# Kernel tuning notes

Measured on AMD Instinct MI355X. Metric: run time of the kernel, lower is better.

Reference implementation:

```python
import jax, jax.numpy as jnp
import numpy as np

NUM_HEADS = 8
KEY_DIM = 64
VALUE_DIM = 64
UPDATE_STEPS_MAX = 3
UPDATE_EPS = 1e-4
LN_EPS = 1e-5


def _layernorm(x, gamma, beta):
    # normalize over last axis (key_dim), per build: shape (..., num_heads, key_dim)
    mu = jnp.mean(x, axis=-1, keepdims=True)
    var = jnp.var(x, axis=-1, keepdims=True)
    return (x - mu) * jax.lax.rsqrt(var + LN_EPS) * gamma + beta


def setup_inputs() -> dict:
    key = jax.random.key(0)
    ks = jax.random.split(key, 8)
    D = 512
    B, S = 8, 1024
    s = 1.0 / np.sqrt(D)
    return {
        "x": jax.random.normal(ks[0], (B, S, D), jnp.float32),
        "Wq": jax.random.normal(ks[1], (D, NUM_HEADS * KEY_DIM), jnp.float32) * s,
        "bq": jnp.zeros((NUM_HEADS * KEY_DIM,), jnp.float32),
        "Wk": jax.random.normal(ks[2], (D, NUM_HEADS * KEY_DIM), jnp.float32) * s,
        "bk": jnp.zeros((NUM_HEADS * KEY_DIM,), jnp.float32),
        "Wv": jax.random.normal(ks[3], (D, NUM_HEADS * VALUE_DIM), jnp.float32) * s,
        "bv": jnp.zeros((NUM_HEADS * VALUE_DIM,), jnp.float32),
        "Wo": jax.random.normal(ks[4], (NUM_HEADS * VALUE_DIM, D), jnp.float32) * s,
        "bo": jnp.zeros((D,), jnp.float32),
        "gamma": jnp.ones((KEY_DIM,), jnp.float32),
        "beta": jnp.zeros((KEY_DIM,), jnp.float32),
    }


def reference(x, Wq, bq, Wk, bk, Wv, bv, Wo, bo, gamma, beta):
    B, S, D = x.shape
    H, dk, dv = NUM_HEADS, KEY_DIM, VALUE_DIM
    # QKV projections -> (B, S, H, d)
    q = (x @ Wq + bq).reshape(B, S, H, dk)
    k = (x @ Wk + bk).reshape(B, S, H, dk)
    v = (x @ Wv + bv).reshape(B, S, H, dv)
    # pattern normalization (LayerNorm over key_dim)
    q = _layernorm(q, gamma, beta)
    k = _layernorm(k, gamma, beta)
    # -> (B, H, S, d)
    q = q.transpose(0, 2, 1, 3)
    k = k.transpose(0, 2, 1, 3)
    v = v.transpose(0, 2, 1, 3)
    scale = jnp.sqrt(jnp.asarray(dk, q.dtype))
    # iterative Hopfield association updates: q <- softmax(qK^T/scale) K
    for _ in range(UPDATE_STEPS_MAX):
        attn = jax.nn.softmax(jnp.einsum("bhqd,bhkd->bhqk", q, k) / scale, axis=-1)
        new_q = jnp.einsum("bhqk,bhkd->bhqd", attn, k)
        diff = jnp.linalg.norm(new_q - q)
        q = jnp.where(diff > UPDATE_EPS, new_q, q)  # eps-gated update
    # final retrieval with values
    attn = jax.nn.softmax(jnp.einsum("bhqd,bhkd->bhqk", q, k) / scale, axis=-1)
    out = jnp.einsum("bhqk,bhkd->bhqd", attn, v)
    out = out.transpose(0, 2, 1, 3).reshape(B, S, H * dv)
    return out @ Wo + bo
```

## Files before the change

kernel.cpp:

```cpp
#include <hip/hip_runtime.h>
#include <stdint.h>


#define DEV static __device__ __forceinline__

typedef __attribute__((ext_vector_type(8))) short short8;
typedef __attribute__((ext_vector_type(8))) __bf16 bf16x8;
typedef __attribute__((ext_vector_type(4))) float f32x4;
typedef __attribute__((ext_vector_type(16))) float f32x16;
typedef __attribute__((ext_vector_type(4))) unsigned int uint4v;

DEV unsigned short f2bf(float f) {
  unsigned int u = __builtin_bit_cast(unsigned int, f);
  u = u + 0x7fffu + ((u >> 16) & 1u);
  return (unsigned short)(u >> 16);
}

DEV unsigned int cvtpk(float lo, float hi) {
  unsigned int r;
  asm("v_cvt_pk_bf16_f32 %0, %1, %2" : "=v"(r) : "v"(lo), "v"(hi));
  return r;
}

DEV f32x4 mfma16(short8 a, short8 b, f32x4 c) {
  return __builtin_amdgcn_mfma_f32_16x16x32_bf16(
      __builtin_bit_cast(bf16x8, a), __builtin_bit_cast(bf16x8, b), c, 0, 0, 0);
}

DEV f32x16 mfma32(short8 a, short8 b, f32x16 c) {
  return __builtin_amdgcn_mfma_f32_32x32x16_bf16(
      __builtin_bit_cast(bf16x8, a), __builtin_bit_cast(bf16x8, b), c, 0, 0, 0);
}

DEV f32x16 zero16() {
  f32x16 z;
#pragma unroll
  for (int i = 0; i < 16; ++i) z[i] = 0.f;
  return z;
}

DEV void gload16(void* lds, const void* g) {
  __builtin_amdgcn_global_load_lds(
      (const __attribute__((address_space(1))) void*)(uintptr_t)g,
      (__attribute__((address_space(3))) void*)(unsigned int)(uintptr_t)lds,
      16, 0, 0);
}

__global__ __launch_bounds__(256)
void xcast_kernel(const float* __restrict__ x, unsigned short* __restrict__ xbf) {
  int i = blockIdx.x * 256 + threadIdx.x;
  float4 v = ((const float4*)x)[i];
  ushort4 o;
  o.x = f2bf(v.x); o.y = f2bf(v.y); o.z = f2bf(v.z); o.w = f2bf(v.w);
  ((ushort4*)xbf)[i] = o;
}

__global__ __launch_bounds__(256)
void wtrans_kernel(const float* __restrict__ Wq, const float* __restrict__ Wk,
                   const float* __restrict__ Wv, const float* __restrict__ Wo,
                   unsigned short* __restrict__ wqkvT, unsigned short* __restrict__ woT) {
  __shared__ float t[64][65];
  int job = blockIdx.x;
  int wsel = job >> 6;
  int tile = job & 63;
  int tr = (tile >> 3) * 64;
  int tc = (tile & 7) * 64;
  const float* W = wsel == 0 ? Wq : wsel == 1 ? Wk : wsel == 2 ? Wv : Wo;
  unsigned short* T = wsel < 3 ? wqkvT + (size_t)wsel * 512 * 512 : woT;
  int lane = threadIdx.x & 63;
  int wv = threadIdx.x >> 6;
  for (int rr = 0; rr < 16; ++rr) {
    int r = wv * 16 + rr;
    t[r][lane] = W[(size_t)(tr + r) * 512 + tc + lane];
  }
  __syncthreads();
  for (int rr = 0; rr < 16; ++rr) {
    int r = wv * 16 + rr;
    T[(size_t)(tc + r) * 512 + tr + lane] = f2bf(t[lane][r]);
  }
}

template <int MODE>
__global__ __launch_bounds__(256, 2)
void gemm_kernel(const unsigned short* __restrict__ A,
                 const unsigned short* __restrict__ WT,
                 const float* __restrict__ b0, const float* __restrict__ b1,
                 const float* __restrict__ b2,
                 const float* __restrict__ gamma, const float* __restrict__ beta,
                 unsigned short* __restrict__ Qo, unsigned short* __restrict__ Ko,
                 unsigned short* __restrict__ Vo, float* __restrict__ Fo) {
  __shared__ __align__(16) unsigned char As[2][16384];
  __shared__ __align__(16) unsigned char Ws[2][16384];

  const int tid = threadIdx.x;
  const int lane = tid & 63;
  const int w = tid >> 6;
  const int l15 = lane & 15;
  const int l4 = lane >> 4;
  const int m0 = blockIdx.x * 128;
  const int by = blockIdx.y;
  const int wm = (w >> 1) * 64;
  const int wn = (w & 1) * 64;

  f32x4 acc[4][4];
#pragma unroll
  for (int mt = 0; mt < 4; ++mt)
#pragma unroll
    for (int nt = 0; nt < 4; ++nt) acc[mt][nt] = (f32x4){0.f, 0.f, 0.f, 0.f};

  auto stage = [&](int i) {
    int buf = i & 1;
    int k0 = i * 64;
#pragma unroll
    for (int it = 0; it < 4; ++it) {
      int idx = it * 256 + tid;
      int row = idx >> 3;
      int sc = ((idx & 7) * 16) ^ ((row & 7) << 4);
      gload16(As[buf] + idx * 16,
              (const unsigned char*)A + ((size_t)(m0 + row) * 512 + k0) * 2 + sc);
      gload16(Ws[buf] + idx * 16,
              (const unsigned char*)WT + ((size_t)(by * 128 + row) * 512 + k0) * 2 + sc);
    }
  };

  stage(0);
  __syncthreads();

  for (int i = 0; i < 8; ++i) {
    int buf = i & 1;
    if (i < 7) stage(i + 1);
    __builtin_amdgcn_s_setprio(1);
#pragma unroll
    for (int kk = 0; kk < 2; ++kk) {
      short8 af[4], bfr[4];
#pragma unroll
      for (int mt = 0; mt < 4; ++mt) {
        int row = wm + mt * 16 + l15;
        int colb = (l4 * 16 + kk * 64) ^ ((row & 7) << 4);
        af[mt] = *(const short8*)(As[buf] + row * 128 + colb);
      }
#pragma unroll
      for (int nt = 0; nt < 4; ++nt) {
        int row = wn + nt * 16 + l15;
        int colb = (l4 * 16 + kk * 64) ^ ((row & 7) << 4);
        bfr[nt] = *(const short8*)(Ws[buf] + row * 128 + colb);
      }
#pragma unroll
      for (int mt = 0; mt < 4; ++mt)
#pragma unroll
        for (int nt = 0; nt < 4; ++nt) acc[mt][nt] = mfma16(af[mt], bfr[nt], acc[mt][nt]);
    }
    __builtin_amdgcn_s_setprio(0);
    __syncthreads();
  }

  const float cs = 1.4426950408889634f / 8.0f;
  const float* bias = (MODE == 1) ? b0 : (by >> 2) == 0 ? b0 : (by >> 2) == 1 ? b1 : b2;
  float bvv[4];
#pragma unroll
  for (int nt = 0; nt < 4; ++nt) bvv[nt] = bias[(by & 3) * 128 + wn + nt * 16 + l15];

  if (MODE == 1) {
#pragma unroll
    for (int mt = 0; mt < 4; ++mt)
#pragma unroll
      for (int r = 0; r < 4; ++r) {
        int gr = m0 + wm + mt * 16 + l4 * 4 + r;
#pragma unroll
        for (int nt = 0; nt < 4; ++nt)
          Fo[(size_t)gr * 512 + (by & 3) * 128 + wn + nt * 16 + l15] =
              acc[mt][nt][r] + bvv[nt];
      }
  } else {
    const int seg = by >> 2;
    const int h = (by & 3) * 2 + (wn >> 6);
    if (seg == 2) {
#pragma unroll
      for (int mt = 0; mt < 4; ++mt)
#pragma unroll
        for (int r = 0; r < 4; ++r) {
          int gr = m0 + wm + mt * 16 + l4 * 4 + r;
          int b = gr >> 10, s = gr & 1023;
          size_t base = ((size_t)(b * 8 + h) << 16) + ((size_t)s << 6);
#pragma unroll
          for (int nt = 0; nt < 4; ++nt)
            Vo[base + nt * 16 + l15] = f2bf(acc[mt][nt][r] + bvv[nt]);
        }
    } else {
      float g4[4], be4[4];
#pragma unroll
      for (int nt = 0; nt < 4; ++nt) {
        g4[nt] = gamma[nt * 16 + l15];
        be4[nt] = beta[nt * 16 + l15];
      }
      unsigned short* dst = seg == 0 ? Qo : Ko;
      const float m = seg == 0 ? cs : 1.0f;
#pragma unroll
      for (int mt = 0; mt < 4; ++mt)
#pragma unroll
        for (int r = 0; r < 4; ++r) {
          float v[4];
#pragma unroll
          for (int nt = 0; nt < 4; ++nt) v[nt] = acc[mt][nt][r] + bvv[nt];
          float s1 = (v[0] + v[1]) + (v[2] + v[3]);
          s1 += __shfl_xor(s1, 1); s1 += __shfl_xor(s1, 2);
          s1 += __shfl_xor(s1, 4); s1 += __shfl_xor(s1, 8);
          float mu = s1 * (1.0f / 64.0f);
          float s2 = v[0]*v[0] + v[1]*v[1] + v[2]*v[2] + v[3]*v[3];
          s2 += __shfl_xor(s2, 1); s2 += __shfl_xor(s2, 2);
          s2 += __shfl_xor(s2, 4); s2 += __shfl_xor(s2, 8);
          float var = s2 * (1.0f / 64.0f) - mu * mu;
          float rs = rsqrtf(var + 1e-5f);
          int gr = m0 + wm + mt * 16 + l4 * 4 + r;
          int b = gr >> 10, s = gr & 1023;
          size_t base = ((size_t)(b * 8 + h) << 16) + ((size_t)s << 6);
#pragma unroll
          for (int nt = 0; nt < 4; ++nt) {
            float y = ((v[nt] - mu) * rs * g4[nt] + be4[nt]) * m;
            dst[base + nt * 16 + l15] = f2bf(y);
          }
        }
    }
  }
}

__global__ __launch_bounds__(256)
void ktrans_kernel(const unsigned short* __restrict__ Kb,
                   const unsigned short* __restrict__ Vb,
                   unsigned short* __restrict__ KTg, unsigned short* __restrict__ VTg) {
  __shared__ unsigned short tile[64][65];
  const int c = blockIdx.x;
  const int bh = blockIdx.y;
  const unsigned short* src = blockIdx.z ? Vb : Kb;
  unsigned short* dst = blockIdx.z ? VTg : KTg;
  const int t = threadIdx.x;
  {
    int j = t >> 2, c16 = (t & 3) * 16;
    const unsigned short* sp = src + ((size_t)bh << 16) + ((size_t)(c * 64 + j) << 6) + c16;
    unsigned short vals[16];
    *(uint4*)(vals) = *(const uint4*)(sp);
    *(uint4*)(vals + 8) = *(const uint4*)(sp + 8);
#pragma unroll
    for (int i = 0; i < 16; ++i) tile[j][c16 + i] = vals[i];
  }
  __syncthreads();
  {
    int d = t >> 2, k16 = (t & 3) * 16;
    unsigned short ov[16];
#pragma unroll
    for (int i = 0; i < 16; ++i) {
      int kp = k16 + i;
      int g = kp >> 5, r5 = kp & 31;
      int c16 = r5 >> 4, h = (r5 >> 3) & 1, ii = r5 & 7;
      int phys = g * 32 + c16 * 16 + 8 * (ii >> 2) + 4 * h + (ii & 3);
      ov[i] = tile[phys][d];
    }
    unsigned short* dp = dst + ((size_t)bh << 16) + ((size_t)d << 10) + c * 64 + k16;
    *(uint4*)(dp) = *(uint4*)(ov);
    *(uint4*)(dp + 8) = *(uint4*)(ov + 8);
  }
}

__global__ __launch_bounds__(256, 2)
void attn_kernel(const unsigned short* __restrict__ Qb,
                 const unsigned short* __restrict__ Kb,
                 const unsigned short* __restrict__ KTg,
                 const unsigned short* __restrict__ VTg,
                 unsigned short* __restrict__ Ob) {
  __shared__ __align__(16) unsigned char Kc[2][8192];
  __shared__ __align__(16) unsigned char Tc[2][8192];

  const int tid = threadIdx.x;
  const int lane = tid & 63;
  const int w = tid >> 6;
  const int l31 = lane & 31;
  const int hi = lane >> 5;
  const int bi = blockIdx.x;
  const int xcd = bi & 7, wnd = bi >> 3;
  const int bh = xcd * 8 + (wnd & 7);
  const int qt = wnd >> 3;
  const int q0 = qt * 128 + w * 32;
  const size_t kvb = (size_t)bh << 17;
  const float cs = 1.4426950408889634f / 8.0f;

  int sOffK[2], sOffT[2];
#pragma unroll
  for (int it = 0; it < 2; ++it) {
    int idx = it * 256 + tid;
    int row = idx >> 3;
    int colb = ((idx & 7) * 16) ^ ((row & 7) << 4);
    sOffK[it] = row * 128 + colb;
    sOffT[it] = row * 2048 + colb;
  }
  const unsigned char* kS = (const unsigned char*)Kb + kvb;
  const unsigned char* tKS = (const unsigned char*)KTg + kvb;
  const unsigned char* tVS = (const unsigned char*)VTg + kvb;

  auto stage = [&](int t) {
    int c = t & 15, buf = t & 1;
    const unsigned char* ts = (t >= 48) ? tVS : tKS;
#pragma unroll
    for (int it = 0; it < 2; ++it) {
      int idx = it * 256 + tid;
      gload16(Kc[buf] + idx * 16, kS + (size_t)c * 8192 + sOffK[it]);
      gload16(Tc[buf] + idx * 16, ts + (size_t)c * 128 + sOffT[it]);
    }
  };

  stage(0);

  short8 qf[4];
  {
    const unsigned char* qp =
        (const unsigned char*)Qb + kvb + ((size_t)(q0 + l31) << 7) + hi * 16;
    qf[0] = *(const short8*)(qp);
    qf[1] = *(const short8*)(qp + 32);
    qf[2] = *(const short8*)(qp + 64);
    qf[3] = *(const short8*)(qp + 96);
  }

  f32x16 acc0 = zero16(), acc1 = zero16();
  float lsum = 0.f;
  const int sw = (l31 & 7) << 4;
  const int hb = hi * 16;
  const int rowA = l31 * 128;

  auto compute = [&](int buf) {
    const unsigned char* KB = Kc[buf];
    const unsigned char* TB = Tc[buf];
    short8 kfa[4], kfb[4];
#pragma unroll
    for (int s = 0; s < 4; ++s) {
      int cb = (32 * s + hb) ^ sw;
      kfa[s] = *(const short8*)(KB + rowA + cb);
      kfb[s] = *(const short8*)(KB + 4096 + rowA + cb);
    }
    f32x16 s0 = zero16(), s1 = zero16();
    __builtin_amdgcn_s_setprio(1);
#pragma unroll
    for (int s = 0; s < 4; ++s) {
      s0 = mfma32(kfa[s], qf[s], s0);
      s1 = mfma32(kfb[s], qf[s], s1);
    }
    __builtin_amdgcn_s_setprio(0);
    unsigned int u0[8], u1[8];
#pragma unroll
    for (int r = 0; r < 16; r += 2) {
      float pA = exp2f(s0[r]), pB = exp2f(s0[r + 1]);
      lsum += pA + pB;
      u0[r >> 1] = cvtpk(pA, pB);
    }
#pragma unroll
    for (int r = 0; r < 16; r += 2) {
      float pA = exp2f(s1[r]), pB = exp2f(s1[r + 1]);
      lsum += pA + pB;
      u1[r >> 1] = cvtpk(pA, pB);
    }
    short8 p00 = __builtin_bit_cast(short8, (uint4v){u0[0], u0[1], u0[2], u0[3]});
    short8 p01 = __builtin_bit_cast(short8, (uint4v){u0[4], u0[5], u0[6], u0[7]});
    short8 p10 = __builtin_bit_cast(short8, (uint4v){u1[0], u1[1], u1[2], u1[3]});
    short8 p11 = __builtin_bit_cast(short8, (uint4v){u1[4], u1[5], u1[6], u1[7]});
    short8 t0, t1;
    __builtin_amdgcn_s_setprio(1);
    t0 = *(const short8*)(TB + rowA + ((0 + hb) ^ sw));
    t1 = *(const short8*)(TB + 4096 + rowA + ((0 + hb) ^ sw));
    acc0 = mfma32(t0, p00, acc0);
    acc1 = mfma32(t1, p00, acc1);
    t0 = *(const short8*)(TB + rowA + ((32 + hb) ^ sw));
    t1 = *(const short8*)(TB + 4096 + rowA + ((32 + hb) ^ sw));
    acc0 = mfma32(t0, p01, acc0);
    acc1 = mfma32(t1, p01, acc1);
    t0 = *(const short8*)(TB + rowA + ((64 + hb) ^ sw));
    t1 = *(const short8*)(TB + 4096 + rowA + ((64 + hb) ^ sw));
    acc0 = mfma32(t0, p10, acc0);
    acc1 = mfma32(t1, p10, acc1);
    t0 = *(const short8*)(TB + rowA + ((96 + hb) ^ sw));
    t1 = *(const short8*)(TB + 4096 + rowA + ((96 + hb) ^ sw));
    acc0 = mfma32(t0, p11, acc0);
    acc1 = mfma32(t1, p11, acc1);
    __builtin_amdgcn_s_setprio(0);
  };

  __syncthreads();

  for (int p = 0; p < 4; ++p) {
    for (int c2 = 0; c2 < 16; c2 += 2) {
      {
        int t = p * 16 + c2;
        if (t < 63) stage(t + 1);
        compute(0);
        __syncthreads();
      }
      {
        int t = p * 16 + c2 + 1;
        if (t < 63) stage(t + 1);
        compute(1);
        __syncthreads();
      }
    }
    lsum += __shfl_xor(lsum, 32);
    if (p < 3) {
      float f = cs / lsum;
#pragma unroll
      for (int s = 0; s < 4; ++s) {
        const f32x16& A = (s >> 1) ? acc1 : acc0;
        const int base = 8 * (s & 1);
        float a0 = A[base] * f, a1 = A[base + 1] * f;
        float a2 = A[base + 2] * f, a3 = A[base + 3] * f;
        float b0 = A[base + 4] * f, b1 = A[base + 5] * f;
        float b2 = A[base + 6] * f, b3 = A[base + 7] * f;
        float s0_ = hi ? a0 : b0, s1_ = hi ? a1 : b1;
        float s2_ = hi ? a2 : b2, s3_ = hi ? a3 : b3;
        float r0 = __shfl_xor(s0_, 32), r1 = __shfl_xor(s1_, 32);
        float r2 = __shfl_xor(s2_, 32), r3 = __shfl_xor(s3_, 32);
        float e0 = hi ? r0 : a0, e1 = hi ? r1 : a1;
        float e2 = hi ? r2 : a2, e3 = hi ? r3 : a3;
        float e4 = hi ? b0 : r0, e5 = hi ? b1 : r1;
        float e6 = hi ? b2 : r2, e7 = hi ? b3 : r3;
        qf[s] = __builtin_bit_cast(
            short8, (uint4v){cvtpk(e0, e1), cvtpk(e2, e3), cvtpk(e4, e5), cvtpk(e6, e7)});
      }
      acc0 = zero16();
      acc1 = zero16();
      lsum = 0.f;
    } else {
      float inv = 1.0f / lsum;
      const int b = bh >> 3, h = bh & 7;
      const int qg = q0 + l31;
      unsigned short* orow = Ob + ((size_t)(b * 1024 + qg) << 9) + h * 64;
#pragma unroll
      for (int dt = 0; dt < 2; ++dt) {
        const f32x16& A = dt ? acc1 : acc0;
#pragma unroll
        for (int rq = 0; rq < 4; ++rq) {
          ushort4 o;
          o.x = f2bf(A[4 * rq + 0] * inv);
          o.y = f2bf(A[4 * rq + 1] * inv);
          o.z = f2bf(A[4 * rq + 2] * inv);
          o.w = f2bf(A[4 * rq + 3] * inv);
          *(ushort4*)(orow + dt * 32 + 8 * rq + 4 * hi) = o;
        }
      }
    }
  }
}

extern "C" void kernel_launch(void* const* d_in, const int* in_sizes, int n_in,
                              void* d_out, int out_size, void* d_ws, size_t ws_size,
                              hipStream_t stream) {
  const float* x  = (const float*)d_in[0];
  const float* Wq = (const float*)d_in[1];
  const float* bq = (const float*)d_in[2];
  const float* Wk = (const float*)d_in[3];
  const float* bk = (const float*)d_in[4];
  const float* Wv = (const float*)d_in[5];
  const float* bv = (const float*)d_in[6];
  const float* Wo = (const float*)d_in[7];
  const float* bo = (const float*)d_in[8];
  const float* gamma = (const float*)d_in[9];
  const float* beta  = (const float*)d_in[10];
  (void)in_sizes; (void)n_in; (void)out_size; (void)ws_size;

  char* ws = (char*)d_ws;
  size_t off = 0;
  auto alloc = [&](size_t bytes) {
    char* p = ws + off;
    off += (bytes + 255) & ~(size_t)255;
    return p;
  };
  unsigned short* xbf   = (unsigned short*)alloc(8192ull * 512 * 2);
  unsigned short* wqkvT = (unsigned short*)alloc(1536ull * 512 * 2);
  unsigned short* woT   = (unsigned short*)alloc(512ull * 512 * 2);
  unsigned short* Qbf   = (unsigned short*)alloc(64ull * 1024 * 64 * 2);
  unsigned short* Kbf   = (unsigned short*)alloc(64ull * 1024 * 64 * 2);
  unsigned short* Vbf   = (unsigned short*)alloc(64ull * 1024 * 64 * 2);
  unsigned short* KTg   = (unsigned short*)alloc(64ull * 1024 * 64 * 2);
  unsigned short* VTg   = (unsigned short*)alloc(64ull * 1024 * 64 * 2);
  unsigned short* Obf   = (unsigned short*)alloc(8192ull * 512 * 2);

  xcast_kernel<<<4096, 256, 0, stream>>>(x, xbf);
  wtrans_kernel<<<256, 256, 0, stream>>>(Wq, Wk, Wv, Wo, wqkvT, woT);

  gemm_kernel<0><<<dim3(64, 12), 256, 0, stream>>>(
      xbf, wqkvT, bq, bk, bv, gamma, beta, Qbf, Kbf, Vbf, nullptr);

  ktrans_kernel<<<dim3(16, 64, 2), 256, 0, stream>>>(Kbf, Vbf, KTg, VTg);

  attn_kernel<<<512, 256, 0, stream>>>(Qbf, Kbf, KTg, VTg, Obf);

  gemm_kernel<1><<<dim3(64, 4), 256, 0, stream>>>(
      Obf, woT, bo, nullptr, nullptr, nullptr, nullptr,
      nullptr, nullptr, nullptr, (float*)d_out);
}
```

Before: 231.5 us.

## Deepen attention pipeline to prefetch two tiles ahead and software-pipeline PV

Measured after the change: 232.5 us. Within noise of the previous version (+0.4%).

```diff
diff --git a/kernel.cpp b/kernel.cpp
--- a/kernel.cpp
+++ b/kernel.cpp
@@ -267,8 +267,8 @@
                  const unsigned short* __restrict__ KTg,
                  const unsigned short* __restrict__ VTg,
                  unsigned short* __restrict__ Ob) {
-  __shared__ __align__(16) unsigned char Kc[2][8192];
-  __shared__ __align__(16) unsigned char Tc[2][8192];
+  __shared__ __align__(16) unsigned char Kc[3][8192];
+  __shared__ __align__(16) unsigned char Tc[4][8192];
 
   const int tid = threadIdx.x;
   const int lane = tid & 63;
@@ -297,17 +297,17 @@
   const unsigned char* tVS = (const unsigned char*)VTg + kvb;
 
   auto stage = [&](int t) {
-    int c = t & 15, buf = t & 1;
+    int c = t & 15;
     const unsigned char* ts = (t >= 48) ? tVS : tKS;
+    unsigned char* kd = Kc[t % 3];
+    unsigned char* td = Tc[t & 3];
 #pragma unroll
     for (int it = 0; it < 2; ++it) {
       int idx = it * 256 + tid;
-      gload16(Kc[buf] + idx * 16, kS + (size_t)c * 8192 + sOffK[it]);
-      gload16(Tc[buf] + idx * 16, ts + (size_t)c * 128 + sOffT[it]);
+      gload16(kd + idx * 16, kS + (size_t)c * 8192 + sOffK[it]);
+      gload16(td + idx * 16, ts + (size_t)c * 128 + sOffT[it]);
     }
   };
-
-  stage(0);
 
   short8 qf[4];
   {
@@ -319,128 +319,148 @@
     qf[3] = *(const short8*)(qp + 96);
   }
 
+  stage(0);
+  stage(1);
+  asm volatile("s_waitcnt vmcnt(4)" ::: "memory");
+  __builtin_amdgcn_s_barrier();
+  __builtin_amdgcn_sched_barrier(0);
+
   f32x16 acc0 = zero16(), acc1 = zero16();
   float lsum = 0.f;
   const int sw = (l31 & 7) << 4;
   const int hb = hi * 16;
   const int rowA = l31 * 128;
 
-  auto compute = [&](int buf) {
-    const unsigned char* KB = Kc[buf];
-    const unsigned char* TB = Tc[buf];
-    short8 kfa[4], kfb[4];
-#pragma unroll
-    for (int s = 0; s < 4; ++s) {
-      int cb = (32 * s + hb) ^ sw;
-      kfa[s] = *(const short8*)(KB + rowA + cb);
-      kfb[s] = *(const short8*)(KB + 4096 + rowA + cb);
-    }
-    f32x16 s0 = zero16(), s1 = zero16();
-    __builtin_amdgcn_s_setprio(1);
-#pragma unroll
-    for (int s = 0; s < 4; ++s) {
-      s0 = mfma32(kfa[s], qf[s], s0);
-      s1 = mfma32(kfb[s], qf[s], s1);
-    }
-    __builtin_amdgcn_s_setprio(0);
-    unsigned int u0[8], u1[8];
-#pragma unroll
-    for (int r = 0; r < 16; r += 2) {
-      float pA = exp2f(s0[r]), pB = exp2f(s0[r + 1]);
-      lsum += pA + pB;
-      u0[r >> 1] = cvtpk(pA, pB);
-    }
-#pragma unroll
-    for (int r = 0; r < 16; r += 2) {
-      float pA = exp2f(s1[r]), pB = exp2f(s1[r + 1]);
-      lsum += pA + pB;
-      u1[r >> 1] = cvtpk(pA, pB);
-    }
-    short8 p00 = __builtin_bit_cast(short8, (uint4v){u0[0], u0[1], u0[2], u0[3]});
-    short8 p01 = __builtin_bit_cast(short8, (uint4v){u0[4], u0[5], u0[6], u0[7]});
-    short8 p10 = __builtin_bit_cast(short8, (uint4v){u1[0], u1[1], u1[2], u1[3]});
-    short8 p11 = __builtin_bit_cast(short8, (uint4v){u1[4], u1[5], u1[6], u1[7]});
+  short8 p0, p1, p2, p3;
+
+  auto PV = [&](int bufT) {
+    const unsigned char* TB = Tc[bufT];
     short8 t0, t1;
-    __builtin_amdgcn_s_setprio(1);
     t0 = *(const short8*)(TB + rowA + ((0 + hb) ^ sw));
     t1 = *(const short8*)(TB + 4096 + rowA + ((0 + hb) ^ sw));
-    acc0 = mfma32(t0, p00, acc0);
-    acc1 = mfma32(t1, p00, acc1);
+    acc0 = mfma32(t0, p0, acc0);
+    acc1 = mfma32(t1, p0, acc1);
     t0 = *(const short8*)(TB + rowA + ((32 + hb) ^ sw));
     t1 = *(const short8*)(TB + 4096 + rowA + ((32 + hb) ^ sw));
-    acc0 = mfma32(t0, p01, acc0);
-    acc1 = mfma32(t1, p01, acc1);
+    acc0 = mfma32(t0, p1, acc0);
+    acc1 = mfma32(t1, p1, acc1);
     t0 = *(const short8*)(TB + rowA + ((64 + hb) ^ sw));
     t1 = *(const short8*)(TB + 4096 + rowA + ((64 + hb) ^ sw));
-    acc0 = mfma32(t0, p10, acc0);
-    acc1 = mfma32(t1, p10, acc1);
+    acc0 = mfma32(t0, p2, acc0);
+    acc1 = mfma32(t1, p2, acc1);
     t0 = *(const short8*)(TB + rowA + ((96 + hb) ^ sw));
     t1 = *(const short8*)(TB + 4096 + rowA + ((96 + hb) ^ sw));
-    acc0 = mfma32(t0, p11, acc0);
-    acc1 = mfma32(t1, p11, acc1);
-    __builtin_amdgcn_s_setprio(0);
+    acc0 = mfma32(t0, p3, acc0);
+    acc1 = mfma32(t1, p3, acc1);
   };
 
-  __syncthreads();
-
-  for (int p = 0; p < 4; ++p) {
-    for (int c2 = 0; c2 < 16; c2 += 2) {
-      {
-        int t = p * 16 + c2;
-        if (t < 63) stage(t + 1);
-        compute(0);
-        __syncthreads();
-      }
-      {
-        int t = p * 16 + c2 + 1;
-        if (t < 63) stage(t + 1);
-        compute(1);
-        __syncthreads();
-      }
-    }
-    lsum += __shfl_xor(lsum, 32);
-    if (p < 3) {
-      float f = cs / lsum;
+  for (int t = 0; t < 64; ++t) {
+    const int c = t & 15;
+    if (t + 2 < 64) stage(t + 2);
+
+    f32x16 s0 = zero16(), s1 = zero16();
+    {
+      const unsigned char* KB = Kc[t % 3];
+      short8 kfa[4], kfb[4];
 #pragma unroll
       for (int s = 0; s < 4; ++s) {
-        const f32x16& A = (s >> 1) ? acc1 : acc0;
-        const int base = 8 * (s & 1);
-        float a0 = A[base] * f, a1 = A[base + 1] * f;
-        float a2 = A[base + 2] * f, a3 = A[base + 3] * f;
-        float b0 = A[base + 4] * f, b1 = A[base + 5] * f;
-        float b2 = A[base + 6] * f, b3 = A[base + 7] * f;
-        float s0_ = hi ? a0 : b0, s1_ = hi ? a1 : b1;
-        float s2_ = hi ? a2 : b2, s3_ = hi ? a3 : b3;
-        float r0 = __shfl_xor(s0_, 32), r1 = __shfl_xor(s1_, 32);
-        float r2 = __shfl_xor(s2_, 32), r3 = __shfl_xor(s3_, 32);
-        float e0 = hi ? r0 : a0, e1 = hi ? r1 : a1;
-        float e2 = hi ? r2 : a2, e3 = hi ? r3 : a3;
-        float e4 = hi ? b0 : r0, e5 = hi ? b1 : r1;
-        float e6 = hi ? b2 : r2, e7 = hi ? b3 : r3;
-        qf[s] = __builtin_bit_cast(
-            short8, (uint4v){cvtpk(e0, e1), cvtpk(e2, e3), cvtpk(e4, e5), cvtpk(e6, e7)});
-      }
-      acc0 = zero16();
-      acc1 = zero16();
-      lsum = 0.f;
-    } else {
-      float inv = 1.0f / lsum;
-      const int b = bh >> 3, h = bh & 7;
-      const int qg = q0 + l31;
-      unsigned short* orow = Ob + ((size_t)(b * 1024 + qg) << 9) + h * 64;
-#pragma unroll
-      for (int dt = 0; dt < 2; ++dt) {
-        const f32x16& A = dt ? acc1 : acc0;
-#pragma unroll
-        for (int rq = 0; rq < 4; ++rq) {
-          ushort4 o;
-          o.x = f2bf(A[4 * rq + 0] * inv);
-          o.y = f2bf(A[4 * rq + 1] * inv);
-          o.z = f2bf(A[4 * rq + 2] * inv);
-          o.w = f2bf(A[4 * rq + 3] * inv);
-          *(ushort4*)(orow + dt * 32 + 8 * rq + 4 * hi) = o;
+        int cb = (32 * s + hb) ^ sw;
+        kfa[s] = *(const short8*)(KB + rowA + cb);
+        kfb[s] = *(const short8*)(KB + 4096 + rowA + cb);
+      }
+      __builtin_amdgcn_s_setprio(1);
+#pragma unroll
+      for (int s = 0; s < 4; ++s) {
+        s0 = mfma32(kfa[s], qf[s], s0);
+        s1 = mfma32(kfb[s], qf[s], s1);
+      }
+      __builtin_amdgcn_s_setprio(0);
+    }
+
+    if (c > 0) {
+      __builtin_amdgcn_s_setprio(1);
+      PV((t - 1) & 3);
+      __builtin_amdgcn_s_setprio(0);
+    }
+
+    {
+      unsigned int u0[8], u1[8];
+#pragma unroll
+      for (int r = 0; r < 16; r += 2) {
+        float pA = exp2f(s0[r]), pB = exp2f(s0[r + 1]);
+        lsum += pA + pB;
+        u0[r >> 1] = cvtpk(pA, pB);
+      }
+#pragma unroll
+      for (int r = 0; r < 16; r += 2) {
+        float pA = exp2f(s1[r]), pB = exp2f(s1[r + 1]);
+        lsum += pA + pB;
+        u1[r >> 1] = cvtpk(pA, pB);
+      }
+      p0 = __builtin_bit_cast(short8, (uint4v){u0[0], u0[1], u0[2], u0[3]});
+      p1 = __builtin_bit_cast(short8, (uint4v){u0[4], u0[5], u0[6], u0[7]});
+      p2 = __builtin_bit_cast(short8, (uint4v){u1[0], u1[1], u1[2], u1[3]});
+      p3 = __builtin_bit_cast(short8, (uint4v){u1[4], u1[5], u1[6], u1[7]});
+    }
+
+    if (c == 15) {
+      __builtin_amdgcn_s_setprio(1);
+      PV(t & 3);
+      __builtin_amdgcn_s_setprio(0);
+      lsum += __shfl_xor(lsum, 32);
+      if (t < 63) {
+        float f = cs / lsum;
+#pragma unroll
+        for (int s = 0; s < 4; ++s) {
+          const f32x16& A = (s >> 1) ? acc1 : acc0;
+          const int base = 8 * (s & 1);
+          float a0 = A[base] * f, a1 = A[base + 1] * f;
+          float a2 = A[base + 2] * f, a3 = A[base + 3] * f;
+          float b0 = A[base + 4] * f, b1 = A[base + 5] * f;
+          float b2 = A[base + 6] * f, b3 = A[base + 7] * f;
+          float s0_ = hi ? a0 : b0, s1_ = hi ? a1 : b1;
+          float s2_ = hi ? a2 : b2, s3_ = hi ? a3 : b3;
+          float r0 = __shfl_xor(s0_, 32), r1 = __shfl_xor(s1_, 32);
+          float r2 = __shfl_xor(s2_, 32), r3 = __shfl_xor(s3_, 32);
+          float e0 = hi ? r0 : a0, e1 = hi ? r1 : a1;
+          float e2 = hi ? r2 : a2, e3 = hi ? r3 : a3;
+          float e4 = hi ? b0 : r0, e5 = hi ? b1 : r1;
+          float e6 = hi ? b2 : r2, e7 = hi ? b3 : r3;
+          qf[s] = __builtin_bit_cast(
+              short8, (uint4v){cvtpk(e0, e1), cvtpk(e2, e3), cvtpk(e4, e5), cvtpk(e6, e7)});
         }
-      }
+        acc0 = zero16();
+        acc1 = zero16();
+        lsum = 0.f;
+      } else {
+        float inv = 1.0f / lsum;
+        const int b = bh >> 3, h = bh & 7;
+        const int qg = q0 + l31;
+        unsigned short* orow = Ob + ((size_t)(b * 1024 + qg) << 9) + h * 64;
+#pragma unroll
+        for (int dt = 0; dt < 2; ++dt) {
+          const f32x16& A = dt ? acc1 : acc0;
+#pragma unroll
+          for (int rq = 0; rq < 4; ++rq) {
+            ushort4 o;
+            o.x = f2bf(A[4 * rq + 0] * inv);
+            o.y = f2bf(A[4 * rq + 1] * inv);
+            o.z = f2bf(A[4 * rq + 2] * inv);
+            o.w = f2bf(A[4 * rq + 3] * inv);
+            *(ushort4*)(orow + dt * 32 + 8 * rq + 4 * hi) = o;
+          }
+        }
+      }
+    }
+
+    if (t < 63) {
+      if (t == 62) {
+        asm volatile("s_waitcnt vmcnt(0)" ::: "memory");
+      } else {
+        asm volatile("s_waitcnt vmcnt(4)" ::: "memory");
+      }
+      __builtin_amdgcn_s_barrier();
+      __builtin_amdgcn_sched_barrier(0);
     }
   }
 }
```

## Load transposed K/V fragments directly from global into registers, stage K in big LDS halves

Applied to the files above, without the earlier changes.

Result: slower. 268.4 us (+16.0%).

```diff
diff --git a/kernel.cpp b/kernel.cpp
--- a/kernel.cpp
+++ b/kernel.cpp
@@ -44,6 +44,21 @@
       (const __attribute__((address_space(1))) void*)(uintptr_t)g,
       (__attribute__((address_space(3))) void*)(unsigned int)(uintptr_t)lds,
       16, 0, 0);
+}
+
+struct TFrag { short8 a0, a1, a2, a3, b0, b1, b2, b3; };
+
+DEV TFrag load_t(const unsigned char* p) {
+  TFrag f;
+  f.a0 = *(const short8*)(p);
+  f.a1 = *(const short8*)(p + 32);
+  f.a2 = *(const short8*)(p + 64);
+  f.a3 = *(const short8*)(p + 96);
+  f.b0 = *(const short8*)(p + 4096);
+  f.b1 = *(const short8*)(p + 4128);
+  f.b2 = *(const short8*)(p + 4160);
+  f.b3 = *(const short8*)(p + 4192);
+  return f;
 }
 
 __global__ __launch_bounds__(256)
@@ -227,12 +242,12 @@
 __global__ __launch_bounds__(256)
 void ktrans_kernel(const unsigned short* __restrict__ Kb,
                    const unsigned short* __restrict__ Vb,
-                   unsigned short* __restrict__ KTg, unsigned short* __restrict__ VTg) {
+                   unsigned short* __restrict__ KTc, unsigned short* __restrict__ VTc) {
   __shared__ unsigned short tile[64][65];
   const int c = blockIdx.x;
   const int bh = blockIdx.y;
   const unsigned short* src = blockIdx.z ? Vb : Kb;
-  unsigned short* dst = blockIdx.z ? VTg : KTg;
+  unsigned short* dst = blockIdx.z ? VTc : KTc;
   const int t = threadIdx.x;
   {
     int j = t >> 2, c16 = (t & 3) * 16;
@@ -255,7 +270,7 @@
       int phys = g * 32 + c16 * 16 + 8 * (ii >> 2) + 4 * h + (ii & 3);
       ov[i] = tile[phys][d];
     }
-    unsigned short* dp = dst + ((size_t)bh << 16) + ((size_t)d << 10) + c * 64 + k16;
+    unsigned short* dp = dst + ((size_t)bh << 16) + c * 4096 + d * 64 + k16;
     *(uint4*)(dp) = *(uint4*)(ov);
     *(uint4*)(dp + 8) = *(uint4*)(ov + 8);
   }
@@ -264,84 +279,79 @@
 __global__ __launch_bounds__(256, 2)
 void attn_kernel(const unsigned short* __restrict__ Qb,
                  const unsigned short* __restrict__ Kb,
-                 const unsigned short* __restrict__ KTg,
-                 const unsigned short* __restrict__ VTg,
+                 const unsigned short* __restrict__ KTc,
+                 const unsigned short* __restrict__ VTc,
                  unsigned short* __restrict__ Ob) {
-  __shared__ __align__(16) unsigned char Kc[2][8192];
-  __shared__ __align__(16) unsigned char Tc[2][8192];
+  __shared__ __align__(16) unsigned char Kc[65536];
 
   const int tid = threadIdx.x;
   const int lane = tid & 63;
   const int w = tid >> 6;
   const int l31 = lane & 31;
   const int hi = lane >> 5;
-  const int bi = blockIdx.x;
-  const int xcd = bi & 7, wnd = bi >> 3;
-  const int bh = xcd * 8 + (wnd & 7);
-  const int qt = wnd >> 3;
+  const int bid = blockIdx.x;
+  const int bh = (bid & 7) * 8 + ((bid >> 3) & 7);
+  const int qt = bid >> 6;
   const int q0 = qt * 128 + w * 32;
   const size_t kvb = (size_t)bh << 17;
   const float cs = 1.4426950408889634f / 8.0f;
 
-  int sOffK[2], sOffT[2];
-#pragma unroll
-  for (int it = 0; it < 2; ++it) {
-    int idx = it * 256 + tid;
-    int row = idx >> 3;
-    int colb = ((idx & 7) * 16) ^ ((row & 7) << 4);
-    sOffK[it] = row * 128 + colb;
-    sOffT[it] = row * 2048 + colb;
-  }
   const unsigned char* kS = (const unsigned char*)Kb + kvb;
-  const unsigned char* tKS = (const unsigned char*)KTg + kvb;
-  const unsigned char* tVS = (const unsigned char*)VTg + kvb;
-
-  auto stage = [&](int t) {
-    int c = t & 15, buf = t & 1;
-    const unsigned char* ts = (t >= 48) ? tVS : tKS;
-#pragma unroll
-    for (int it = 0; it < 2; ++it) {
+  const int tlane = l31 * 128 + hi * 16;
+  const unsigned char* tKl = (const unsigned char*)KTc + kvb + tlane;
+  const unsigned char* tVl = (const unsigned char*)VTc + kvb + tlane;
+
+  auto stageK = [&](int h) {
+    const unsigned char* s = kS + h * 65536;
+#pragma unroll
+    for (int it = 0; it < 16; ++it) {
       int idx = it * 256 + tid;
-      gload16(Kc[buf] + idx * 16, kS + (size_t)c * 8192 + sOffK[it]);
-      gload16(Tc[buf] + idx * 16, ts + (size_t)c * 128 + sOffT[it]);
+      int row = idx >> 3;
+      int colb = ((idx & 7) * 16) ^ ((row & 7) << 4);
+      gload16(Kc + idx * 16, s + row * 128 + colb);
     }
   };
 
-  stage(0);
-
+  const int sw = (l31 & 7) << 4;
+  const int hb = hi * 16;
+  const int rowA = l31 * 128;
+  const int ko0 = rowA + ((0 + hb) ^ sw);
+  const int ko1 = rowA + ((32 + hb) ^ sw);
+  const int ko2 = rowA + ((64 + hb) ^ sw);
+  const int ko3 = rowA + ((96 + hb) ^ sw);
+
+  stageK(0);
   short8 qf[4];
   {
     const unsigned char* qp =
-        (const unsigned char*)Qb + kvb + ((size_t)(q0 + l31) << 7) + hi * 16;
+        (const unsigned char*)Qb + kvb + (size_t)(q0 + l31) * 128 + hb;
     qf[0] = *(const short8*)(qp);
     qf[1] = *(const short8*)(qp + 32);
     qf[2] = *(const short8*)(qp + 64);
     qf[3] = *(const short8*)(qp + 96);
   }
+  asm volatile("s_waitcnt vmcnt(0)" ::: "memory");
+  __builtin_amdgcn_s_barrier();
 
   f32x16 acc0 = zero16(), acc1 = zero16();
   float lsum = 0.f;
-  const int sw = (l31 & 7) << 4;
-  const int hb = hi * 16;
-  const int rowA = l31 * 128;
-
-  auto compute = [&](int buf) {
-    const unsigned char* KB = Kc[buf];
-    const unsigned char* TB = Tc[buf];
-    short8 kfa[4], kfb[4];
-#pragma unroll
-    for (int s = 0; s < 4; ++s) {
-      int cb = (32 * s + hb) ^ sw;
-      kfa[s] = *(const short8*)(KB + rowA + cb);
-      kfb[s] = *(const short8*)(KB + 4096 + rowA + cb);
-    }
+  TFrag tA = load_t(tKl), tB;
+
+  auto compute = [&](int cb, const TFrag& tf) {
+    short8 ka0 = *(const short8*)(Kc + cb + ko0);
+    short8 ka1 = *(const short8*)(Kc + cb + ko1);
+    short8 ka2 = *(const short8*)(Kc + cb + ko2);
+    short8 ka3 = *(const short8*)(Kc + cb + ko3);
+    short8 kb0 = *(const short8*)(Kc + cb + 4096 + ko0);
+    short8 kb1 = *(const short8*)(Kc + cb + 4096 + ko1);
+    short8 kb2 = *(const short8*)(Kc + cb + 4096 + ko2);
+    short8 kb3 = *(const short8*)(Kc + cb + 4096 + ko3);
     f32x16 s0 = zero16(), s1 = zero16();
     __builtin_amdgcn_s_setprio(1);
-#pragma unroll
-    for (int s = 0; s < 4; ++s) {
-      s0 = mfma32(kfa[s], qf[s], s0);
-      s1 = mfma32(kfb[s], qf[s], s1);
-    }
+    s0 = mfma32(ka0, qf[0], s0); s1 = mfma32(kb0, qf[0], s1);
+    s0 = mfma32(ka1, qf[1], s0); s1 = mfma32(kb1, qf[1], s1);
+    s0 = mfma32(ka2, qf[2], s0); s1 = mfma32(kb2, qf[2], s1);
+    s0 = mfma32(ka3, qf[3], s0); s1 = mfma32(kb3, qf[3], s1);
     __builtin_amdgcn_s_setprio(0);
     unsigned int u0[8], u1[8];
 #pragma unroll
@@ -356,46 +366,42 @@
       lsum += pA + pB;
       u1[r >> 1] = cvtpk(pA, pB);
     }
-    short8 p00 = __builtin_bit_cast(short8, (uint4v){u0[0], u0[1], u0[2], u0[3]});
-    short8 p01 = __builtin_bit_cast(short8, (uint4v){u0[4], u0[5], u0[6], u0[7]});
-    short8 p10 = __builtin_bit_cast(short8, (uint4v){u1[0], u1[1], u1[2], u1[3]});
-    short8 p11 = __builtin_bit_cast(short8, (uint4v){u1[4], u1[5], u1[6], u1[7]});
-    short8 t0, t1;
+    short8 p0 = __builtin_bit_cast(short8, (uint4v){u0[0], u0[1], u0[2], u0[3]});
+    short8 p1 = __builtin_bit_cast(short8, (uint4v){u0[4], u0[5], u0[6], u0[7]});
+    short8 p2 = __builtin_bit_cast(short8, (uint4v){u1[0], u1[1], u1[2], u1[3]});
+    short8 p3 = __builtin_bit_cast(short8, (uint4v){u1[4], u1[5], u1[6], u1[7]});
     __builtin_amdgcn_s_setprio(1);
-    t0 = *(const short8*)(TB + rowA + ((0 + hb) ^ sw));
-    t1 = *(const short8*)(TB + 4096 + rowA + ((0 + hb) ^ sw));
-    acc0 = mfma32(t0, p00, acc0);
-    acc1 = mfma32(t1, p00, acc1);
-    t0 = *(const short8*)(TB + rowA + ((32 + hb) ^ sw));
-    t1 = *(const short8*)(TB + 4096 + rowA + ((32 + hb) ^ sw));
-    acc0 = mfma32(t0, p01, acc0);
-    acc1 = mfma32(t1, p01, acc1);
-    t0 = *(const short8*)(TB + rowA + ((64 + hb) ^ sw));
-    t1 = *(const short8*)(TB + 4096 + rowA + ((64 + hb) ^ sw));
-    acc0 = mfma32(t0, p10, acc0);
-    acc1 = mfma32(t1, p10, acc1);
-    t0 = *(const short8*)(TB + rowA + ((96 + hb) ^ sw));
-    t1 = *(const short8*)(TB + 4096 + rowA + ((96 + hb) ^ sw));
-    acc0 = mfma32(t0, p11, acc0);
-    acc1 = mfma32(t1, p11, acc1);
+    acc0 = mfma32(tf.a0, p0, acc0); acc1 = mfma32(tf.b0, p0, acc1);
+    acc0 = mfma32(tf.a1, p1, acc0); acc1 = mfma32(tf.b1, p1, acc1);
+    acc0 = mfma32(tf.a2, p2, acc0); acc1 = mfma32(tf.b2, p2, acc1);
+    acc0 = mfma32(tf.a3, p3, acc0); acc1 = mfma32(tf.b3, p3, acc1);
     __builtin_amdgcn_s_setprio(0);
   };
 
-  __syncthreads();
-
   for (int p = 0; p < 4; ++p) {
-    for (int c2 = 0; c2 < 16; c2 += 2) {
-      {
-        int t = p * 16 + c2;
-        if (t < 63) stage(t + 1);
-        compute(0);
-        __syncthreads();
-      }
-      {
-        int t = p * 16 + c2 + 1;
-        if (t < 63) stage(t + 1);
-        compute(1);
-        __syncthreads();
+    for (int h = 0; h < 2; ++h) {
+      if (p | h) {
+        __builtin_amdgcn_s_barrier();
+        stageK(h);
+        asm volatile("s_waitcnt vmcnt(0)" ::: "memory");
+        __builtin_amdgcn_s_barrier();
+      }
+      for (int cc = 0; cc < 8; cc += 2) {
+        const int g = p * 16 + h * 8 + cc;
+        {
+          const int tg = g + 1;
+          const unsigned char* ns = (tg >= 48 && tg < 64) ? tVl : tKl;
+          tB = load_t(ns + ((tg & 15) << 13));
+          __builtin_amdgcn_sched_barrier(0);
+          compute(cc * 8192, tA);
+        }
+        {
+          const int tg = g + 2;
+          const unsigned char* ns = (tg >= 48 && tg < 64) ? tVl : tKl;
+          tA = load_t(ns + ((tg & 15) << 13));
+          __builtin_amdgcn_sched_barrier(0);
+          compute(cc * 8192 + 8192, tB);
+        }
       }
     }
     lsum += __shfl_xor(lsum, 32);
@@ -425,9 +431,9 @@
       lsum = 0.f;
     } else {
       float inv = 1.0f / lsum;
-      const int b = bh >> 3, h = bh & 7;
+      const int b = bh >> 3, h8 = bh & 7;
       const int qg = q0 + l31;
-      unsigned short* orow = Ob + ((size_t)(b * 1024 + qg) << 9) + h * 64;
+      unsigned short* orow = Ob + ((size_t)(b * 1024 + qg) << 9) + h8 * 64;
 #pragma unroll
       for (int dt = 0; dt < 2; ++dt) {
         const f32x16& A = dt ? acc1 : acc0;
@@ -474,8 +480,8 @@
   unsigned short* Qbf   = (unsigned short*)alloc(64ull * 1024 * 64 * 2);
   unsigned short* Kbf   = (unsigned short*)alloc(64ull * 1024 * 64 * 2);
   unsigned short* Vbf   = (unsigned short*)alloc(64ull * 1024 * 64 * 2);
-  unsigned short* KTg   = (unsigned short*)alloc(64ull * 1024 * 64 * 2);
-  unsigned short* VTg   = (unsigned short*)alloc(64ull * 1024 * 64 * 2);
+  unsigned short* KTc   = (unsigned short*)alloc(64ull * 1024 * 64 * 2);
+  unsigned short* VTc   = (unsigned short*)alloc(64ull * 1024 * 64 * 2);
   unsigned short* Obf   = (unsigned short*)alloc(8192ull * 512 * 2);
 
   xcast_kernel<<<4096, 256, 0, stream>>>(x, xbf);
@@ -484,9 +490,9 @@
   gemm_kernel<0><<<dim3(64, 12), 256, 0, stream>>>(
       xbf, wqkvT, bq, bk, bv, gamma, beta, Qbf, Kbf, Vbf, nullptr);
 
-  ktrans_kernel<<<dim3(16, 64, 2), 256, 0, stream>>>(Kbf, Vbf, KTg, VTg);
-
-  attn_kernel<<<512, 256, 0, stream>>>(Qbf, Kbf, KTg, VTg, Obf);
+  ktrans_kernel<<<dim3(16, 64, 2), 256, 0, stream>>>(Kbf, Vbf, KTc, VTc);
+
+  attn_kernel<<<512, 256, 0, stream>>>(Qbf, Kbf, KTc, VTc, Obf);
 
   gemm_kernel<1><<<dim3(64, 4), 256, 0, stream>>>(
       Obf, woT, bo, nullptr, nullptr, nullptr, nullptr,
```
